# Kernel tuning notes

Measured on AMD Instinct MI355X. Metric: run time of the kernel, lower is better.

## Reference

```python
import jax, jax.numpy as jnp
import numpy as np

N_NODES = 50000
N_EDGES = 800000
IN_CH = 512
HID = 128
OUT_CH = 2
N_GRAPHS = 64
EPS = 1e-5


def _gcn_conv(x, src, dst, W, b):
    # GCNConv: out = D^-1/2 (A + I) D^-1/2 (x W) + b  (PyG semantics, self-loops added)
    n = x.shape[0]
    h = x @ W  # [N, H]
    loop = jnp.arange(n)
    src2 = jnp.concatenate([src, loop])
    dst2 = jnp.concatenate([dst, loop])
    deg = jax.ops.segment_sum(jnp.ones_like(dst2, dtype=h.dtype), dst2, num_segments=n)
    dinv = jax.lax.rsqrt(deg)  # deg >= 1 due to self-loops
    norm = dinv[src2] * dinv[dst2]  # [E+N]
    msg = h[src2] * norm[:, None]  # gather + normalize
    out = jax.ops.segment_sum(msg, dst2, num_segments=n)  # scatter-add
    return out + b


def _batchnorm_eval(x, gamma, beta, rm, rv):
    return (x - rm) * jax.lax.rsqrt(rv + EPS) * gamma + beta


def setup_inputs() -> dict:
    key = jax.random.key(0)
    ks = jax.random.split(key, 16)
    x = jax.random.normal(ks[0], (N_NODES, IN_CH), dtype=jnp.float32)
    edge_index = jax.random.randint(ks[1], (2, N_EDGES), 0, N_NODES, dtype=jnp.int64)
    batch = jnp.sort(jax.random.randint(ks[2], (N_NODES,), 0, N_GRAPHS, dtype=jnp.int64))
    s1 = 1.0 / np.sqrt(IN_CH)
    s2 = 1.0 / np.sqrt(HID)
    return {
        'x': x,
        'edge_index': edge_index,
        'batch': batch,
        'W1': jax.random.normal(ks[3], (IN_CH, HID), dtype=jnp.float32) * s1,
        'b1': jnp.zeros((HID,), dtype=jnp.float32),
        'gamma1': jax.random.normal(ks[4], (HID,), dtype=jnp.float32) * 0.1 + 1.0,
        'beta1': jax.random.normal(ks[5], (HID,), dtype=jnp.float32) * 0.1,
        'rm1': jax.random.normal(ks[6], (HID,), dtype=jnp.float32) * 0.1,
        'rv1': jax.random.uniform(ks[7], (HID,), dtype=jnp.float32, minval=0.5, maxval=1.5),
        'W2': jax.random.normal(ks[8], (HID, HID), dtype=jnp.float32) * s2,
        'b2': jnp.zeros((HID,), dtype=jnp.float32),
        'gamma2': jax.random.normal(ks[9], (HID,), dtype=jnp.float32) * 0.1 + 1.0,
        'beta2': jax.random.normal(ks[10], (HID,), dtype=jnp.float32) * 0.1,
        'rm2': jax.random.normal(ks[11], (HID,), dtype=jnp.float32) * 0.1,
        'rv2': jax.random.uniform(ks[12], (HID,), dtype=jnp.float32, minval=0.5, maxval=1.5),
        'Wl': jax.random.normal(ks[13], (HID, OUT_CH), dtype=jnp.float32) * s2,
        'bl': jnp.zeros((OUT_CH,), dtype=jnp.float32),
    }


def reference(x, edge_index, batch, W1, b1, gamma1, beta1, rm1, rv1,
              W2, b2, gamma2, beta2, rm2, rv2, Wl, bl):
    # Eval mode: BatchNorm uses running stats; dropout is identity.
    src, dst = edge_index[0], edge_index[1]
    h = _gcn_conv(x, src, dst, W1, b1)
    h = jax.nn.relu(_batchnorm_eval(h, gamma1, beta1, rm1, rv1))
    h = _gcn_conv(h, src, dst, W2, b2)
    h = jax.nn.relu(_batchnorm_eval(h, gamma2, beta2, rm2, rv2))
    # global mean pool over graphs in the batch
    sums = jax.ops.segment_sum(h, batch, num_segments=N_GRAPHS)  # [G, H]
    counts = jax.ops.segment_sum(jnp.ones((h.shape[0],), dtype=h.dtype), batch, num_segments=N_GRAPHS)
    pooled = sums / jnp.maximum(counts, 1.0)[:, None]
    return pooled @ Wl + bl  # [G, OUT_CH]
```

## Files before the change

kernel.cpp:

```cpp
#include <hip/hip_runtime.h>

#define EPSV 1e-5f

typedef __attribute__((ext_vector_type(8))) short short8;
typedef __attribute__((ext_vector_type(4))) float f32x4;
typedef unsigned int uint;
typedef unsigned short ushort;

__global__ __launch_bounds__(256) void init_k(int* __restrict__ cnt,
                                              const int* __restrict__ batch,
                                              int* __restrict__ gstart,
                                              int nnodes, int ngraphs) {
    int i = blockIdx.x * 256 + threadIdx.x;
    if (i < nnodes) cnt[i] = 0;
    if (blockIdx.x == 0 && threadIdx.x <= ngraphs) {
        int g = threadIdx.x;
        int lo = 0, hi = nnodes;
        while (lo < hi) {
            int mid = (lo + hi) >> 1;
            if (batch[mid] < g) lo = mid + 1; else hi = mid;
        }
        gstart[g] = lo;
    }
}

__global__ __launch_bounds__(256) void degcount_k(const int* __restrict__ dst,
                                                  int* __restrict__ cnt,
                                                  int nedges) {
    int i = blockIdx.x * 256 + threadIdx.x;
    if (i < nedges) atomicAdd(&cnt[dst[i]], 1);
}

__global__ __launch_bounds__(256) void scan1_k(const int* __restrict__ cnt,
                                               int* __restrict__ rowptr,
                                               int* __restrict__ bsum,
                                               float* __restrict__ dinv, int n) {
    __shared__ int sh[256];
    const int tx = threadIdx.x;
    const int base = blockIdx.x * 1024;
    int v[4];
    int s = 0;
#pragma unroll
    for (int j = 0; j < 4; j++) {
        int idx = base + tx * 4 + j;
        v[j] = (idx < n) ? cnt[idx] : 0;
        if (idx < n) dinv[idx] = rsqrtf(1.0f + (float)v[j]);
        s += v[j];
    }
    sh[tx] = s;
    __syncthreads();
#pragma unroll
    for (int off = 1; off < 256; off <<= 1) {
        int t = (tx >= off) ? sh[tx - off] : 0;
        __syncthreads();
        sh[tx] += t;
        __syncthreads();
    }
    int run = sh[tx] - s;
#pragma unroll
    for (int j = 0; j < 4; j++) {
        int idx = base + tx * 4 + j;
        if (idx < n) rowptr[idx] = run;
        run += v[j];
    }
    if (tx == 255) bsum[blockIdx.x] = sh[255];
}

__global__ __launch_bounds__(64) void scan2_k(int* __restrict__ bsum, int nb) {
    __shared__ int sh[64];
    const int tx = threadIdx.x;
    int v = (tx < nb) ? bsum[tx] : 0;
    sh[tx] = v;
    __syncthreads();
#pragma unroll
    for (int off = 1; off < 64; off <<= 1) {
        int t = (tx >= off) ? sh[tx - off] : 0;
        __syncthreads();
        sh[tx] += t;
        __syncthreads();
    }
    if (tx < nb) bsum[tx] = sh[tx] - v;
}

__global__ __launch_bounds__(256) void scan3_k(int* __restrict__ rowptr,
                                               int* __restrict__ cur,
                                               const int* __restrict__ bsum,
                                               int n, int nedges) {
    const int tx = threadIdx.x;
    const int base = blockIdx.x * 1024;
    int off = bsum[blockIdx.x];
#pragma unroll
    for (int j = 0; j < 4; j++) {
        int idx = base + tx * 4 + j;
        if (idx < n) {
            int r = rowptr[idx] + off;
            rowptr[idx] = r;
            cur[idx] = r;
        }
    }
    if (blockIdx.x == 0 && tx == 0) rowptr[n] = nedges;
}

__global__ __launch_bounds__(256) void fill_k(const int* __restrict__ src,
                                              const int* __restrict__ dst,
                                              int* __restrict__ cur,
                                              int* __restrict__ esrc, int nedges) {
    int i = blockIdx.x * 256 + threadIdx.x;
    if (i >= nedges) return;
    int pos = atomicAdd(&cur[dst[i]], 1);
    esrc[pos] = src[i];
}

__global__ __launch_bounds__(256) void wprep_k(const float* __restrict__ W1,
                                               const float* __restrict__ W2,
                                               ushort* __restrict__ wt1,
                                               ushort* __restrict__ wt2) {
    int i = blockIdx.x * 256 + threadIdx.x;
    if (i < 512 * 128) {
        int k = i >> 7, c = i & 127;
        unsigned u = __builtin_bit_cast(unsigned, W1[i]);
        wt1[c * 512 + k] = (ushort)((u + 0x7fffu + ((u >> 16) & 1u)) >> 16);
    } else if (i < 512 * 128 + 128 * 128) {
        int j = i - 512 * 128;
        int k = j >> 7, c = j & 127;
        unsigned u = __builtin_bit_cast(unsigned, W2[j]);
        wt2[c * 128 + k] = (ushort)((u + 0x7fffu + ((u >> 16) & 1u)) >> 16);
    }
}

template <int K>
__global__ __launch_bounds__(256) void gemm_mfma_k(const float* __restrict__ X,
                                                   const ushort* __restrict__ wT,
                                                   const float* __restrict__ dinv,
                                                   float* __restrict__ H,
                                                   ushort* __restrict__ hb16,
                                                   int nrows) {
    __shared__ float  lAs[2][64 * 64];
    __shared__ ushort lBs[2][128 * 64];

    const int tx = threadIdx.x;
    const int wu = __builtin_amdgcn_readfirstlane(tx >> 6);
    const int l = tx & 63;
    const int lrow = l & 15;
    const int kgrp = l >> 4;
    const int rowB = blockIdx.x * 64;
    const int row0 = rowB + wu * 16;

    f32x4 acc[8];
#pragma unroll
    for (int g = 0; g < 8; g++) acc[g] = (f32x4){0.f, 0.f, 0.f, 0.f};

    auto STAGE = [&](int buf, int k0) {
#pragma unroll
        for (int q = 0; q < 4; q++) {
            int j = wu * 4 + q;
            int row = j * 4 + (l >> 4);
            int slot = l & 15;
            int grow = rowB + row;
            if (grow >= nrows) grow = nrows - 1;
            const float* src = X + (size_t)grow * K + k0 + ((slot ^ (row & 15)) * 4);
            float* dst = &lAs[buf][j * 256];
            __builtin_amdgcn_global_load_lds(
                (const __attribute__((address_space(1))) unsigned int*)(const void*)src,
                (__attribute__((address_space(3))) unsigned int*)(void*)dst,
                16, 0, 0);
        }
#pragma unroll
        for (int q = 0; q < 4; q++) {
            int j = wu * 4 + q;
            int col = j * 8 + (l >> 3);
            int slot = l & 7;
            const ushort* src = wT + (size_t)col * K + k0 + ((slot ^ (col & 7)) * 8);
            ushort* dst = &lBs[buf][j * 512];
            __builtin_amdgcn_global_load_lds(
                (const __attribute__((address_space(1))) unsigned int*)(const void*)src,
                (__attribute__((address_space(3))) unsigned int*)(void*)dst,
                16, 0, 0);
        }
    };

    constexpr int NIT = K / 64;

    STAGE(0, 0);

#pragma unroll
    for (int i = 0; i < NIT; i++) {
        asm volatile("s_waitcnt vmcnt(0)" ::: "memory");
        __builtin_amdgcn_s_barrier();
        __builtin_amdgcn_sched_barrier(0);

        if (i + 1 < NIT) STAGE((i + 1) & 1, (i + 1) * 64);
        asm volatile("" ::: "memory");

        const int buf = i & 1;
        const int trow = wu * 16 + lrow;
#pragma unroll
        for (int ks = 0; ks < 2; ks++) {
            int s16 = (ks * 4 + kgrp) * 2;
            f32x4 a0 = *reinterpret_cast<const f32x4*>(
                &lAs[buf][trow * 64 + ((s16 ^ lrow) & 15) * 4]);
            f32x4 a1 = *reinterpret_cast<const f32x4*>(
                &lAs[buf][trow * 64 + (((s16 + 1) ^ lrow) & 15) * 4]);
            short8 ah, al;
#pragma unroll
            for (int j = 0; j < 8; j++) {
                float f = (j < 4) ? a0[j] : a1[j - 4];
                unsigned u = __builtin_bit_cast(unsigned, f);
                ah[j] = (short)(u >> 16);
                float hif = __builtin_bit_cast(float, u & 0xffff0000u);
                float lof = f - hif;
                al[j] = (short)(__builtin_bit_cast(unsigned, lof) >> 16);
            }
#pragma unroll
            for (int g = 0; g < 8; g++) {
                int cc = g * 16 + lrow;
                int phys = (ks * 4 + kgrp) ^ (cc & 7);
                short8 bb = *reinterpret_cast<const short8*>(
                    &lBs[buf][cc * 64 + phys * 8]);
                acc[g] = __builtin_amdgcn_mfma_f32_16x16x32_bf16(ah, bb, acc[g], 0, 0, 0);
                acc[g] = __builtin_amdgcn_mfma_f32_16x16x32_bf16(al, bb, acc[g], 0, 0, 0);
            }
        }
    }

#pragma unroll
    for (int r = 0; r < 4; r++) {
        int row = row0 + kgrp * 4 + r;
        if (row < nrows) {
            float dn = dinv[row];
            float* hrow = H + (size_t)row * 128 + lrow;
            ushort* hbrow = hb16 + (size_t)row * 128 + lrow;
#pragma unroll
            for (int g = 0; g < 8; g++) {
                float v = acc[g][r];
                hrow[g * 16] = v;
                unsigned u = __builtin_bit_cast(unsigned, v * dn);
                hbrow[g * 16] = (ushort)((u + 0x7fffu + ((u >> 16) & 1u)) >> 16);
            }
        }
    }
}

__global__ __launch_bounds__(256) void agg_k(const float* __restrict__ H,
                                             const uint* __restrict__ hb,
                                             const int* __restrict__ rowptr,
                                             const int* __restrict__ esrc,
                                             const float* __restrict__ dinv,
                                             const float* __restrict__ bias,
                                             const float* __restrict__ gamma,
                                             const float* __restrict__ beta,
                                             const float* __restrict__ rm,
                                             const float* __restrict__ rv,
                                             float* __restrict__ OUT,
                                             int nnodes) {
    int node = blockIdx.x * 4 + (threadIdx.x >> 6);
    if (node >= nnodes) return;
    node = __builtin_amdgcn_readfirstlane(node);
    const int l = threadIdx.x & 63;
    const int c = l * 2;
    const float dn = dinv[node];
    const int beg = rowptr[node], end = rowptr[node + 1];

    float2 hv = *reinterpret_cast<const float2*>(H + (size_t)node * 128 + c);
    float ax0 = hv.x * dn, ay0 = hv.y * dn;
    float ax1 = 0.f, ay1 = 0.f, ax2 = 0.f, ay2 = 0.f, ax3 = 0.f, ay3 = 0.f;
    const uint* hbl = hb + l;

    int j = beg;
    for (; j + 3 < end; j += 4) {
        int s0 = esrc[j], s1 = esrc[j + 1], s2 = esrc[j + 2], s3 = esrc[j + 3];
        uint u0 = hbl[(size_t)s0 * 64];
        uint u1 = hbl[(size_t)s1 * 64];
        uint u2 = hbl[(size_t)s2 * 64];
        uint u3 = hbl[(size_t)s3 * 64];
        ax0 += __builtin_bit_cast(float, u0 << 16);
        ay0 += __builtin_bit_cast(float, u0 & 0xffff0000u);
        ax1 += __builtin_bit_cast(float, u1 << 16);
        ay1 += __builtin_bit_cast(float, u1 & 0xffff0000u);
        ax2 += __builtin_bit_cast(float, u2 << 16);
        ay2 += __builtin_bit_cast(float, u2 & 0xffff0000u);
        ax3 += __builtin_bit_cast(float, u3 << 16);
        ay3 += __builtin_bit_cast(float, u3 & 0xffff0000u);
    }
    for (; j < end; j++) {
        uint u0 = hbl[(size_t)esrc[j] * 64];
        ax0 += __builtin_bit_cast(float, u0 << 16);
        ay0 += __builtin_bit_cast(float, u0 & 0xffff0000u);
    }
    float accx = (ax0 + ax1) + (ax2 + ax3);
    float accy = (ay0 + ay1) + (ay2 + ay3);

    float v0 = accx * dn + bias[c];
    float v1 = accy * dn + bias[c + 1];
    v0 = (v0 - rm[c])     * rsqrtf(rv[c] + EPSV)     * gamma[c]     + beta[c];
    v1 = (v1 - rm[c + 1]) * rsqrtf(rv[c + 1] + EPSV) * gamma[c + 1] + beta[c + 1];
    v0 = fmaxf(v0, 0.0f);
    v1 = fmaxf(v1, 0.0f);

    *reinterpret_cast<float2*>(OUT + (size_t)node * 128 + c) = make_float2(v0, v1);
}

__global__ __launch_bounds__(256) void pool1_k(const float* __restrict__ V,
                                               const int* __restrict__ gstart,
                                               float* __restrict__ partial) {
    __shared__ float sh[256];
    const int g = blockIdx.x >> 5;
    const int p = blockIdx.x & 31;
    const int tx = threadIdx.x;
    const int ch = tx & 127;
    const int sub = tx >> 7;
    const int beg = gstart[g], end = gstart[g + 1];
    const int chunk = (end - beg + 31) >> 5;
    const int s = beg + p * chunk;
    const int e = min(s + chunk, end);
    float acc = 0.0f;
    for (int i = s + sub; i < e; i += 2)
        acc += V[(size_t)i * 128 + ch];
    sh[tx] = acc;
    __syncthreads();
    if (tx < 128)
        partial[(size_t)blockIdx.x * 128 + tx] = sh[tx] + sh[tx + 128];
}

__global__ __launch_bounds__(128) void pool2_k(const float* __restrict__ partial,
                                               const int* __restrict__ gstart,
                                               float* __restrict__ pooled) {
    const int g = blockIdx.x;
    const int ch = threadIdx.x;
    float s = 0.0f;
#pragma unroll
    for (int p = 0; p < 32; p++)
        s += partial[(size_t)((g << 5) + p) * 128 + ch];
    float cnt = fmaxf((float)(gstart[g + 1] - gstart[g]), 1.0f);
    pooled[g * 128 + ch] = s / cnt;
}

__global__ __launch_bounds__(128) void final_k(const float* __restrict__ pooled,
                                               const float* __restrict__ Wl,
                                               const float* __restrict__ bl,
                                               float* __restrict__ out) {
    int tx = threadIdx.x;
    int g = tx >> 1, o = tx & 1;
    float s = 0.0f;
#pragma unroll 8
    for (int c = 0; c < 128; c++) s += pooled[g * 128 + c] * Wl[c * 2 + o];
    out[tx] = s + bl[o];
}

extern "C" void kernel_launch(void* const* d_in, const int* in_sizes, int n_in,
                              void* d_out, int out_size, void* d_ws, size_t ws_size,
                              hipStream_t stream) {
    const float* x      = (const float*)d_in[0];
    const int*   ei     = (const int*)d_in[1];
    const int*   batch  = (const int*)d_in[2];
    const float* W1     = (const float*)d_in[3];
    const float* b1     = (const float*)d_in[4];
    const float* gamma1 = (const float*)d_in[5];
    const float* beta1  = (const float*)d_in[6];
    const float* rm1    = (const float*)d_in[7];
    const float* rv1    = (const float*)d_in[8];
    const float* W2     = (const float*)d_in[9];
    const float* b2     = (const float*)d_in[10];
    const float* gamma2 = (const float*)d_in[11];
    const float* beta2  = (const float*)d_in[12];
    const float* rm2    = (const float*)d_in[13];
    const float* rv2    = (const float*)d_in[14];
    const float* Wl     = (const float*)d_in[15];
    const float* bl     = (const float*)d_in[16];
    float* out = (float*)d_out;

    const int nnodes  = in_sizes[2];
    const int nedges  = in_sizes[1] / 2;
    const int ngraphs = 64;
    const int* srcp = ei;
    const int* dstp = ei + nedges;

    float* wsA     = (float*)d_ws;
    float* wsB     = wsA + (size_t)nnodes * 128;
    float* dinv    = wsB + (size_t)nnodes * 128;
    float* pooled  = dinv + nnodes;
    float* partial = pooled + 64 * 128;
    int*   cnt     = (int*)(partial + 64 * 32 * 128);
    int*   rowptr  = cnt + nnodes;
    int*   cur     = rowptr + nnodes + 1;
    int*   bsum    = cur + nnodes;
    int*   gstart  = bsum + 64;
    int*   esrc    = gstart + 65;
    uintptr_t wp   = ((uintptr_t)(esrc + nedges) + 15) & ~(uintptr_t)15;
    ushort* wt1  = (ushort*)wp;
    ushort* wt2  = wt1 + 512 * 128;
    ushort* hb16 = wt2 + 128 * 128;
    uint*   hb   = (uint*)hb16;

    dim3 blk(256);
    const int gNodes = (nnodes + 255) / 256;
    const int gEdges = (nedges + 255) / 256;
    const int gGemm  = (nnodes + 63) / 64;
    const int gAgg   = (nnodes + 3) / 4;
    const int nScanB = (nnodes + 1023) / 1024;

    init_k<<<gNodes, blk, 0, stream>>>(cnt, batch, gstart, nnodes, ngraphs);
    wprep_k<<<(512 * 128 + 128 * 128 + 255) / 256, blk, 0, stream>>>(W1, W2, wt1, wt2);
    degcount_k<<<gEdges, blk, 0, stream>>>(dstp, cnt, nedges);
    scan1_k<<<nScanB, blk, 0, stream>>>(cnt, rowptr, bsum, dinv, nnodes);
    scan2_k<<<1, 64, 0, stream>>>(bsum, nScanB);
    scan3_k<<<nScanB, blk, 0, stream>>>(rowptr, cur, bsum, nnodes, nedges);
    fill_k<<<gEdges, blk, 0, stream>>>(srcp, dstp, cur, esrc, nedges);

    gemm_mfma_k<512><<<gGemm, blk, 0, stream>>>(x, wt1, dinv, wsA, hb16, nnodes);
    agg_k<<<gAgg, blk, 0, stream>>>(wsA, hb, rowptr, esrc, dinv, b1, gamma1, beta1,
                                    rm1, rv1, wsB, nnodes);

    gemm_mfma_k<128><<<gGemm, blk, 0, stream>>>(wsB, wt2, dinv, wsA, hb16, nnodes);
    agg_k<<<gAgg, blk, 0, stream>>>(wsA, hb, rowptr, esrc, dinv, b2, gamma2, beta2,
                                    rm2, rv2, wsB, nnodes);

    pool1_k<<<ngraphs * 32, blk, 0, stream>>>(wsB, gstart, partial);
    pool2_k<<<ngraphs, 128, 0, stream>>>(partial, gstart, pooled);
    final_k<<<1, 128, 0, stream>>>(pooled, Wl, bl, out);
}
```

Measured before the change: 258.5 us.

## Drop fp32 H buffer, fuse weight prep and final linear, unroll aggregation

The GEMM no longer writes an fp32 copy of H. The aggregation now reads the self-loop term from the bf16 pre-scaled buffer, which cuts about 25 MB of writes plus the matching reads per layer. Weight conversion is merged into init_k, and the final linear layer is folded into pool2_k with a shared-memory reduction, removing two launches. The gather loop is unrolled to 8 with a 2-wide remainder to keep more loads in flight. Reading the self term in bf16 adds a small precision loss.

```diff
diff --git a/kernel.cpp b/kernel.cpp
--- a/kernel.cpp
+++ b/kernel.cpp
@@ -10,9 +10,23 @@
 __global__ __launch_bounds__(256) void init_k(int* __restrict__ cnt,
                                               const int* __restrict__ batch,
                                               int* __restrict__ gstart,
+                                              const float* __restrict__ W1,
+                                              const float* __restrict__ W2,
+                                              ushort* __restrict__ wt1,
+                                              ushort* __restrict__ wt2,
                                               int nnodes, int ngraphs) {
     int i = blockIdx.x * 256 + threadIdx.x;
     if (i < nnodes) cnt[i] = 0;
+    if (i < 512 * 128) {
+        int k = i >> 7, c = i & 127;
+        unsigned u = __builtin_bit_cast(unsigned, W1[i]);
+        wt1[c * 512 + k] = (ushort)((u + 0x7fffu + ((u >> 16) & 1u)) >> 16);
+    } else if (i < 512 * 128 + 128 * 128) {
+        int j = i - 512 * 128;
+        int k = j >> 7, c = j & 127;
+        unsigned u = __builtin_bit_cast(unsigned, W2[j]);
+        wt2[c * 128 + k] = (ushort)((u + 0x7fffu + ((u >> 16) & 1u)) >> 16);
+    }
     if (blockIdx.x == 0 && threadIdx.x <= ngraphs) {
         int g = threadIdx.x;
         int lo = 0, hi = nnodes;
@@ -111,28 +125,10 @@
     esrc[pos] = src[i];
 }
 
-__global__ __launch_bounds__(256) void wprep_k(const float* __restrict__ W1,
-                                               const float* __restrict__ W2,
-                                               ushort* __restrict__ wt1,
-                                               ushort* __restrict__ wt2) {
-    int i = blockIdx.x * 256 + threadIdx.x;
-    if (i < 512 * 128) {
-        int k = i >> 7, c = i & 127;
-        unsigned u = __builtin_bit_cast(unsigned, W1[i]);
-        wt1[c * 512 + k] = (ushort)((u + 0x7fffu + ((u >> 16) & 1u)) >> 16);
-    } else if (i < 512 * 128 + 128 * 128) {
-        int j = i - 512 * 128;
-        int k = j >> 7, c = j & 127;
-        unsigned u = __builtin_bit_cast(unsigned, W2[j]);
-        wt2[c * 128 + k] = (ushort)((u + 0x7fffu + ((u >> 16) & 1u)) >> 16);
-    }
-}
-
 template <int K>
 __global__ __launch_bounds__(256) void gemm_mfma_k(const float* __restrict__ X,
                                                    const ushort* __restrict__ wT,
                                                    const float* __restrict__ dinv,
-                                                   float* __restrict__ H,
                                                    ushort* __restrict__ hb16,
                                                    int nrows) {
     __shared__ float  lAs[2][64 * 64];
@@ -228,21 +224,17 @@
         int row = row0 + kgrp * 4 + r;
         if (row < nrows) {
             float dn = dinv[row];
-            float* hrow = H + (size_t)row * 128 + lrow;
             ushort* hbrow = hb16 + (size_t)row * 128 + lrow;
 #pragma unroll
             for (int g = 0; g < 8; g++) {
-                float v = acc[g][r];
-                hrow[g * 16] = v;
-                unsigned u = __builtin_bit_cast(unsigned, v * dn);
+                unsigned u = __builtin_bit_cast(unsigned, acc[g][r] * dn);
                 hbrow[g * 16] = (ushort)((u + 0x7fffu + ((u >> 16) & 1u)) >> 16);
             }
         }
     }
 }
 
-__global__ __launch_bounds__(256) void agg_k(const float* __restrict__ H,
-                                             const uint* __restrict__ hb,
+__global__ __launch_bounds__(256) void agg_k(const uint* __restrict__ hb,
                                              const int* __restrict__ rowptr,
                                              const int* __restrict__ esrc,
                                              const float* __restrict__ dinv,
@@ -260,19 +252,25 @@
     const int c = l * 2;
     const float dn = dinv[node];
     const int beg = rowptr[node], end = rowptr[node + 1];
-
-    float2 hv = *reinterpret_cast<const float2*>(H + (size_t)node * 128 + c);
-    float ax0 = hv.x * dn, ay0 = hv.y * dn;
+    const uint* hbl = hb + l;
+
+    uint us = hbl[(size_t)node * 64];
+    float ax0 = __builtin_bit_cast(float, us << 16);
+    float ay0 = __builtin_bit_cast(float, us & 0xffff0000u);
     float ax1 = 0.f, ay1 = 0.f, ax2 = 0.f, ay2 = 0.f, ax3 = 0.f, ay3 = 0.f;
-    const uint* hbl = hb + l;
 
     int j = beg;
-    for (; j + 3 < end; j += 4) {
-        int s0 = esrc[j], s1 = esrc[j + 1], s2 = esrc[j + 2], s3 = esrc[j + 3];
+    for (; j + 7 < end; j += 8) {
+        int s0 = esrc[j],     s1 = esrc[j + 1], s2 = esrc[j + 2], s3 = esrc[j + 3];
+        int s4 = esrc[j + 4], s5 = esrc[j + 5], s6 = esrc[j + 6], s7 = esrc[j + 7];
         uint u0 = hbl[(size_t)s0 * 64];
         uint u1 = hbl[(size_t)s1 * 64];
         uint u2 = hbl[(size_t)s2 * 64];
         uint u3 = hbl[(size_t)s3 * 64];
+        uint u4 = hbl[(size_t)s4 * 64];
+        uint u5 = hbl[(size_t)s5 * 64];
+        uint u6 = hbl[(size_t)s6 * 64];
+        uint u7 = hbl[(size_t)s7 * 64];
         ax0 += __builtin_bit_cast(float, u0 << 16);
         ay0 += __builtin_bit_cast(float, u0 & 0xffff0000u);
         ax1 += __builtin_bit_cast(float, u1 << 16);
@@ -281,8 +279,25 @@
         ay2 += __builtin_bit_cast(float, u2 & 0xffff0000u);
         ax3 += __builtin_bit_cast(float, u3 << 16);
         ay3 += __builtin_bit_cast(float, u3 & 0xffff0000u);
-    }
-    for (; j < end; j++) {
+        ax0 += __builtin_bit_cast(float, u4 << 16);
+        ay0 += __builtin_bit_cast(float, u4 & 0xffff0000u);
+        ax1 += __builtin_bit_cast(float, u5 << 16);
+        ay1 += __builtin_bit_cast(float, u5 & 0xffff0000u);
+        ax2 += __builtin_bit_cast(float, u6 << 16);
+        ay2 += __builtin_bit_cast(float, u6 & 0xffff0000u);
+        ax3 += __builtin_bit_cast(float, u7 << 16);
+        ay3 += __builtin_bit_cast(float, u7 & 0xffff0000u);
+    }
+    for (; j + 1 < end; j += 2) {
+        int s0 = esrc[j], s1 = esrc[j + 1];
+        uint u0 = hbl[(size_t)s0 * 64];
+        uint u1 = hbl[(size_t)s1 * 64];
+        ax0 += __builtin_bit_cast(float, u0 << 16);
+        ay0 += __builtin_bit_cast(float, u0 & 0xffff0000u);
+        ax1 += __builtin_bit_cast(float, u1 << 16);
+        ay1 += __builtin_bit_cast(float, u1 & 0xffff0000u);
+    }
+    if (j < end) {
         uint u0 = hbl[(size_t)esrc[j] * 64];
         ax0 += __builtin_bit_cast(float, u0 << 16);
         ay0 += __builtin_bit_cast(float, u0 & 0xffff0000u);
@@ -324,7 +339,10 @@
 
 __global__ __launch_bounds__(128) void pool2_k(const float* __restrict__ partial,
                                                const int* __restrict__ gstart,
-                                               float* __restrict__ pooled) {
+                                               const float* __restrict__ Wl,
+                                               const float* __restrict__ bl,
+                                               float* __restrict__ out) {
+    __shared__ float s0[128], s1[128];
     const int g = blockIdx.x;
     const int ch = threadIdx.x;
     float s = 0.0f;
@@ -332,19 +350,19 @@
     for (int p = 0; p < 32; p++)
         s += partial[(size_t)((g << 5) + p) * 128 + ch];
     float cnt = fmaxf((float)(gstart[g + 1] - gstart[g]), 1.0f);
-    pooled[g * 128 + ch] = s / cnt;
-}
-
-__global__ __launch_bounds__(128) void final_k(const float* __restrict__ pooled,
-                                               const float* __restrict__ Wl,
-                                               const float* __restrict__ bl,
-                                               float* __restrict__ out) {
-    int tx = threadIdx.x;
-    int g = tx >> 1, o = tx & 1;
-    float s = 0.0f;
-#pragma unroll 8
-    for (int c = 0; c < 128; c++) s += pooled[g * 128 + c] * Wl[c * 2 + o];
-    out[tx] = s + bl[o];
+    float pooled = s / cnt;
+    s0[ch] = pooled * Wl[ch * 2];
+    s1[ch] = pooled * Wl[ch * 2 + 1];
+    __syncthreads();
+#pragma unroll
+    for (int off = 64; off > 0; off >>= 1) {
+        if (ch < off) { s0[ch] += s0[ch + off]; s1[ch] += s1[ch + off]; }
+        __syncthreads();
+    }
+    if (ch == 0) {
+        out[g * 2]     = s0[0] + bl[0];
+        out[g * 2 + 1] = s1[0] + bl[1];
+    }
 }
 
 extern "C" void kernel_launch(void* const* d_in, const int* in_sizes, int n_in,
@@ -375,11 +393,9 @@
     const int* srcp = ei;
     const int* dstp = ei + nedges;
 
-    float* wsA     = (float*)d_ws;
-    float* wsB     = wsA + (size_t)nnodes * 128;
+    float* wsB     = (float*)d_ws;
     float* dinv    = wsB + (size_t)nnodes * 128;
-    float* pooled  = dinv + nnodes;
-    float* partial = pooled + 64 * 128;
+    float* partial = dinv + nnodes;
     int*   cnt     = (int*)(partial + 64 * 32 * 128);
     int*   rowptr  = cnt + nnodes;
     int*   cur     = rowptr + nnodes + 1;
@@ -398,24 +414,24 @@
     const int gGemm  = (nnodes + 63) / 64;
     const int gAgg   = (nnodes + 3) / 4;
     const int nScanB = (nnodes + 1023) / 1024;
-
-    init_k<<<gNodes, blk, 0, stream>>>(cnt, batch, gstart, nnodes, ngraphs);
-    wprep_k<<<(512 * 128 + 128 * 128 + 255) / 256, blk, 0, stream>>>(W1, W2, wt1, wt2);
+    const int gInit  = max(gNodes, (512 * 128 + 128 * 128 + 255) / 256);
+
+    init_k<<<gInit, blk, 0, stream>>>(cnt, batch, gstart, W1, W2, wt1, wt2,
+                                      nnodes, ngraphs);
     degcount_k<<<gEdges, blk, 0, stream>>>(dstp, cnt, nedges);
     scan1_k<<<nScanB, blk, 0, stream>>>(cnt, rowptr, bsum, dinv, nnodes);
     scan2_k<<<1, 64, 0, stream>>>(bsum, nScanB);
     scan3_k<<<nScanB, blk, 0, stream>>>(rowptr, cur, bsum, nnodes, nedges);
     fill_k<<<gEdges, blk, 0, stream>>>(srcp, dstp, cur, esrc, nedges);
 
-    gemm_mfma_k<512><<<gGemm, blk, 0, stream>>>(x, wt1, dinv, wsA, hb16, nnodes);
-    agg_k<<<gAgg, blk, 0, stream>>>(wsA, hb, rowptr, esrc, dinv, b1, gamma1, beta1,
+    gemm_mfma_k<512><<<gGemm, blk, 0, stream>>>(x, wt1, dinv, hb16, nnodes);
+    agg_k<<<gAgg, blk, 0, stream>>>(hb, rowptr, esrc, dinv, b1, gamma1, beta1,
                                     rm1, rv1, wsB, nnodes);
 
-    gemm_mfma_k<128><<<gGemm, blk, 0, stream>>>(wsB, wt2, dinv, wsA, hb16, nnodes);
-    agg_k<<<gAgg, blk, 0, stream>>>(wsA, hb, rowptr, esrc, dinv, b2, gamma2, beta2,
+    gemm_mfma_k<128><<<gGemm, blk, 0, stream>>>(wsB, wt2, dinv, hb16, nnodes);
+    agg_k<<<gAgg, blk, 0, stream>>>(hb, rowptr, esrc, dinv, b2, gamma2, beta2,
                                     rm2, rv2, wsB, nnodes);
 
     pool1_k<<<ngraphs * 32, blk, 0, stream>>>(wsB, gstart, partial);
-    pool2_k<<<ngraphs, 128, 0, stream>>>(partial, gstart, pooled);
-    final_k<<<1, 128, 0, stream>>>(pooled, Wl, bl, out);
-}
+    pool2_k<<<ngraphs, 128, 0, stream>>>(partial, gstart, Wl, bl, out);
+}
```

Measured after the change: 233.5 us. 9.7% less time.
